# Performance work log

Measured on AMD Instinct MI355X. Metric: run time of the kernel, lower is better.

Reference implementation:

```python
import jax, jax.numpy as jnp
import numpy as np

B, N, F, K = 4096, 2048, 64, 64


def setup_inputs() -> dict:
    key = jax.random.key(0)
    k1, k2, k3, k4, k5 = jax.random.split(key, 5)
    X = jax.random.normal(k1, (B, N), dtype=jnp.float32)
    W = jax.random.normal(k2, (1, N), dtype=jnp.float32) * (1.0 / np.sqrt(N))
    b = jax.random.normal(k3, (1,), dtype=jnp.float32)
    vector = jax.random.normal(k4, (N, F, K), dtype=jnp.float32)
    feature2field = jax.random.randint(k5, (N,), 0, F, dtype=jnp.int32)
    return {"X": X, "W": W, "b": b, "vector": vector, "feature2field": feature2field}


def reference(X, W, b, vector, feature2field):
    # linear part: [B, 1]
    linear = X @ W.T + b
    # field-aware latent vector of feature i w.r.t. its own field: V[i] = vector[i, f2f[i]]  -> [N, K]
    V = vector[jnp.arange(vector.shape[0]), feature2field]
    # pairwise latent dot products S[i,j] = <V[i], V[j]>  -> [N, N]
    S = V @ V.T
    # Gram matrix over batch: P[i,j] = sum_b X[b,i] * X[b,j]  -> [N, N]
    P = X.T @ X
    # original loop accumulates sum over i<j and over batch of S[i,j] * X[:,i]*X[:,j],
    # then adds that scalar to every row of the linear output
    triu = jnp.triu(jnp.ones_like(S), k=1)
    interaction = jnp.sum(S * P * triu)
    return linear + interaction
```

## Files before the change

### kernel.cpp

```cpp
#include <hip/hip_runtime.h>

#define NB 4096
#define NN 2048
#define NF 64
#define NK 64

#define RPB   16
#define TPB   1024
#define NWAVE 16
#define CPW   (NN / NWAVE)
#define KS    (CPW / 32)
#define GRID  (NB / RPB)

typedef short bf16x8 __attribute__((ext_vector_type(8)));
typedef float f32x4  __attribute__((ext_vector_type(4)));

#define OFF_VGTH 0
#define OFF_VGTL (OFF_VGTH + NK * NN * 2)
#define OFF_VN   (OFF_VGTL + NK * NN * 2)
#define OFF_LINT (OFF_VN + NN * 4)
#define OFF_STOT (OFF_LINT + NB * 4)

__device__ inline unsigned short bf16_rtn(float f) {
    unsigned u = __float_as_uint(f);
    return (unsigned short)((u + 0x7fffu + ((u >> 16) & 1u)) >> 16);
}

__global__ __launch_bounds__(256) void k_prep(const float* __restrict__ vec,
                                              const int* __restrict__ f2f,
                                              unsigned short* __restrict__ VgTh,
                                              unsigned short* __restrict__ VgTl,
                                              float* __restrict__ vnorm,
                                              float* __restrict__ stot) {
    __shared__ unsigned short tH[64][72];
    __shared__ unsigned short tL[64][72];
    const int t  = threadIdx.x;
    const int i0 = blockIdx.x * 64;
    if (blockIdx.x == 0 && t == 0) *stot = 0.f;
    {
        const int il = t >> 2;
        const int sg = (t & 3) * 16;
        const int i  = i0 + il;
        const int f  = f2f[i];
        const float* p = vec + (size_t)i * (NF * NK) + (size_t)f * NK + sg;
        float nsum = 0.f;
        #pragma unroll
        for (int j4 = 0; j4 < 4; ++j4) {
            float4 v = *reinterpret_cast<const float4*>(p + j4 * 4);
            float vv[4] = {v.x, v.y, v.z, v.w};
            #pragma unroll
            for (int e = 0; e < 4; ++e) {
                float x = vv[e];
                nsum = fmaf(x, x, nsum);
                unsigned xb = __float_as_uint(x);
                float hf = __uint_as_float(xb & 0xffff0000u);
                int k = sg + j4 * 4 + e;
                tH[il][k] = (unsigned short)(xb >> 16);
                tL[il][k] = bf16_rtn(x - hf);
            }
        }
        nsum += __shfl_xor(nsum, 1, 64);
        nsum += __shfl_xor(nsum, 2, 64);
        if ((t & 3) == 0) vnorm[i] = nsum;
    }
    __syncthreads();
    {
        const int k  = t >> 2;
        const int is = (t & 3) * 16;
        unsigned short hb[16], lb[16];
        #pragma unroll
        for (int j = 0; j < 16; ++j) { hb[j] = tH[is + j][k]; lb[j] = tL[is + j][k]; }
        unsigned short* ph = VgTh + (size_t)k * NN + i0 + is;
        unsigned short* pl = VgTl + (size_t)k * NN + i0 + is;
        *reinterpret_cast<uint4*>(ph)     = *reinterpret_cast<uint4*>(hb);
        *reinterpret_cast<uint4*>(ph + 8) = *reinterpret_cast<uint4*>(hb + 8);
        *reinterpret_cast<uint4*>(pl)     = *reinterpret_cast<uint4*>(lb);
        *reinterpret_cast<uint4*>(pl + 8) = *reinterpret_cast<uint4*>(lb + 8);
    }
}

__global__ __launch_bounds__(TPB, 4) void k_main(const float* __restrict__ X,
                                                 const float* __restrict__ Wg,
                                                 const unsigned short* __restrict__ VgTh,
                                                 const unsigned short* __restrict__ VgTl,
                                                 const float* __restrict__ vn,
                                                 float* __restrict__ lint,
                                                 float* __restrict__ stot) {
    __shared__ float Tl[NWAVE * 1088];
    __shared__ float linW[NWAVE * 17];
    __shared__ float ddW[NWAVE * 17];
    __shared__ float rowRes[RPB];

    const int t    = threadIdx.x;
    const int w    = t >> 6;
    const int lane = t & 63;
    const int m    = lane & 15;
    const int quad = lane >> 4;
    const int r0   = blockIdx.x * RPB;
    const int row  = r0 + m;
    const int cw   = w * CPW;

    const float* xp = X  + (size_t)row * NN + cw + quad * 8;
    const float* wp = Wg + cw + quad * 8;
    const float* np = vn + cw + quad * 8;
    const unsigned short* bhp = VgTh + (size_t)m * NN + cw + quad * 8;
    const unsigned short* blp = VgTl + (size_t)m * NN + cw + quad * 8;

    f32x4 acc[4];
    #pragma unroll
    for (int nt = 0; nt < 4; ++nt)
        #pragma unroll
        for (int e = 0; e < 4; ++e) acc[nt][e] = 0.f;
    float lin = 0.f, dd = 0.f;

    #pragma unroll
    for (int s = 0; s < KS; ++s) {
        float4 xa = *reinterpret_cast<const float4*>(xp + s * 32);
        float4 xb = *reinterpret_cast<const float4*>(xp + s * 32 + 4);
        float4 wa = *reinterpret_cast<const float4*>(wp + s * 32);
        float4 wb = *reinterpret_cast<const float4*>(wp + s * 32 + 4);
        float4 na = *reinterpret_cast<const float4*>(np + s * 32);
        float4 nb = *reinterpret_cast<const float4*>(np + s * 32 + 4);

        float xs8[8] = {xa.x, xa.y, xa.z, xa.w, xb.x, xb.y, xb.z, xb.w};
        float ws8[8] = {wa.x, wa.y, wa.z, wa.w, wb.x, wb.y, wb.z, wb.w};
        float ns8[8] = {na.x, na.y, na.z, na.w, nb.x, nb.y, nb.z, nb.w};

        #pragma unroll
        for (int j = 0; j < 8; ++j) {
            lin = fmaf(xs8[j], ws8[j], lin);
            dd  = fmaf(xs8[j] * xs8[j], ns8[j], dd);
        }

        bf16x8 ah, al;
        #pragma unroll
        for (int j = 0; j < 8; ++j) {
            unsigned ub = __float_as_uint(xs8[j]);
            ah[j] = (short)(ub >> 16);
            float hf = __uint_as_float(ub & 0xffff0000u);
            al[j] = (short)bf16_rtn(xs8[j] - hf);
        }

        #pragma unroll
        for (int nt = 0; nt < 4; ++nt) {
            bf16x8 bh = *reinterpret_cast<const bf16x8*>(bhp + (size_t)nt * 16 * NN + s * 32);
            bf16x8 bl = *reinterpret_cast<const bf16x8*>(blp + (size_t)nt * 16 * NN + s * 32);
            acc[nt] = __builtin_amdgcn_mfma_f32_16x16x32_bf16(ah, bh, acc[nt], 0, 0, 0);
            acc[nt] = __builtin_amdgcn_mfma_f32_16x16x32_bf16(al, bh, acc[nt], 0, 0, 0);
            acc[nt] = __builtin_amdgcn_mfma_f32_16x16x32_bf16(ah, bl, acc[nt], 0, 0, 0);
        }
    }

    #pragma unroll
    for (int nt = 0; nt < 4; ++nt)
        #pragma unroll
        for (int r = 0; r < 4; ++r)
            Tl[w * 1088 + (quad * 4 + r) * 68 + nt * 16 + m] = acc[nt][r];

    lin += __shfl_xor(lin, 16, 64); lin += __shfl_xor(lin, 32, 64);
    dd  += __shfl_xor(dd, 16, 64);  dd  += __shfl_xor(dd, 32, 64);
    if (quad == 0) { linW[w * 17 + m] = lin; ddW[w * 17 + m] = dd; }
    __syncthreads();

    {
        float ts = 0.f;
        #pragma unroll
        for (int ww = 0; ww < NWAVE; ++ww)
            ts += Tl[ww * 1088 + w * 68 + lane];
        float s2 = ts * ts;
        #pragma unroll
        for (int d = 1; d < 64; d <<= 1) s2 += __shfl_xor(s2, d, 64);
        float lw = (lane < 16) ? linW[lane * 17 + w] : 0.f;
        float dw = (lane < 16) ? ddW [lane * 17 + w] : 0.f;
        #pragma unroll
        for (int d = 1; d < 16; d <<= 1) {
            lw += __shfl_xor(lw, d, 64);
            dw += __shfl_xor(dw, d, 64);
        }
        if (lane == 0) {
            lint[r0 + w] = lw;
            rowRes[w]    = s2 - dw;
        }
    }
    __syncthreads();

    if (t == 0) {
        float p = 0.f;
        #pragma unroll
        for (int r = 0; r < RPB; ++r) p += rowRes[r];
        atomicAdd(stot, p);
    }
}

__global__ __launch_bounds__(256) void k_final(const float* __restrict__ lint,
                                               const float* __restrict__ stot,
                                               const float* __restrict__ bptr,
                                               float* __restrict__ out) {
    int b = blockIdx.x * 256 + threadIdx.x;
    out[b] = lint[b] + bptr[0] + 0.5f * stot[0];
}

extern "C" void kernel_launch(void* const* d_in, const int* in_sizes, int n_in,
                              void* d_out, int out_size, void* d_ws, size_t ws_size,
                              hipStream_t stream) {
    const float* X    = (const float*)d_in[0];
    const float* W    = (const float*)d_in[1];
    const float* bias = (const float*)d_in[2];
    const float* vec  = (const float*)d_in[3];
    const int*   f2f  = (const int*)d_in[4];
    float* out = (float*)d_out;

    char* base = (char*)d_ws;
    unsigned short* VgTh = (unsigned short*)(base + OFF_VGTH);
    unsigned short* VgTl = (unsigned short*)(base + OFF_VGTL);
    float* vnorm = (float*)(base + OFF_VN);
    float* lint  = (float*)(base + OFF_LINT);
    float* stot  = (float*)(base + OFF_STOT);

    k_prep<<<NN / 64, 256, 0, stream>>>(vec, f2f, VgTh, VgTl, vnorm, stot);
    k_main<<<GRID, TPB, 0, stream>>>(X, W, VgTh, VgTl, vnorm, lint, stot);
    k_final<<<NB / 256, 256, 0, stream>>>(lint, stot, bias, out);
}
```

Baseline: 118.5 us.

## Pre-swizzle V into MFMA fragment layout so B-operand loads are contiguous

```diff
diff --git a/kernel.cpp b/kernel.cpp
--- a/kernel.cpp
+++ b/kernel.cpp
@@ -15,9 +15,8 @@
 typedef short bf16x8 __attribute__((ext_vector_type(8)));
 typedef float f32x4  __attribute__((ext_vector_type(4)));
 
-#define OFF_VGTH 0
-#define OFF_VGTL (OFF_VGTH + NK * NN * 2)
-#define OFF_VN   (OFF_VGTL + NK * NN * 2)
+#define OFF_VGF  0
+#define OFF_VN   (OFF_VGF + 64 * 8 * 512 * 2)
 #define OFF_LINT (OFF_VN + NN * 4)
 #define OFF_STOT (OFF_LINT + NB * 4)
 
@@ -28,8 +27,7 @@
 
 __global__ __launch_bounds__(256) void k_prep(const float* __restrict__ vec,
                                               const int* __restrict__ f2f,
-                                              unsigned short* __restrict__ VgTh,
-                                              unsigned short* __restrict__ VgTl,
+                                              unsigned short* __restrict__ VgF,
                                               float* __restrict__ vnorm,
                                               float* __restrict__ stot) {
     __shared__ unsigned short tH[64][72];
@@ -65,24 +63,28 @@
     }
     __syncthreads();
     {
-        const int k  = t >> 2;
-        const int is = (t & 3) * 16;
+        const int r   = t >> 2;
+        const int seg = t & 3;
+        const int S   = blockIdx.x * 2 + (seg >> 1);
+        const int q1  = (seg & 1) * 2;
         unsigned short hb[16], lb[16];
         #pragma unroll
-        for (int j = 0; j < 16; ++j) { hb[j] = tH[is + j][k]; lb[j] = tL[is + j][k]; }
-        unsigned short* ph = VgTh + (size_t)k * NN + i0 + is;
-        unsigned short* pl = VgTl + (size_t)k * NN + i0 + is;
-        *reinterpret_cast<uint4*>(ph)     = *reinterpret_cast<uint4*>(hb);
-        *reinterpret_cast<uint4*>(ph + 8) = *reinterpret_cast<uint4*>(hb + 8);
-        *reinterpret_cast<uint4*>(pl)     = *reinterpret_cast<uint4*>(lb);
-        *reinterpret_cast<uint4*>(pl + 8) = *reinterpret_cast<uint4*>(lb + 8);
+        for (int u = 0; u < 16; ++u) {
+            hb[u] = tH[seg * 16 + u][r];
+            lb[u] = tL[seg * 16 + u][r];
+        }
+        unsigned short* d = VgF + ((size_t)S * 8 + (r >> 4) * 2) * 512
+                                + ((r & 15) * 4 + q1) * 8;
+        *reinterpret_cast<uint4*>(d)            = *reinterpret_cast<uint4*>(hb);
+        *reinterpret_cast<uint4*>(d + 8)        = *reinterpret_cast<uint4*>(hb + 8);
+        *reinterpret_cast<uint4*>(d + 512)      = *reinterpret_cast<uint4*>(lb);
+        *reinterpret_cast<uint4*>(d + 512 + 8)  = *reinterpret_cast<uint4*>(lb + 8);
     }
 }
 
 __global__ __launch_bounds__(TPB, 4) void k_main(const float* __restrict__ X,
                                                  const float* __restrict__ Wg,
-                                                 const unsigned short* __restrict__ VgTh,
-                                                 const unsigned short* __restrict__ VgTl,
+                                                 const unsigned short* __restrict__ VgF,
                                                  const float* __restrict__ vn,
                                                  float* __restrict__ lint,
                                                  float* __restrict__ stot) {
@@ -103,8 +105,7 @@
     const float* xp = X  + (size_t)row * NN + cw + quad * 8;
     const float* wp = Wg + cw + quad * 8;
     const float* np = vn + cw + quad * 8;
-    const unsigned short* bhp = VgTh + (size_t)m * NN + cw + quad * 8;
-    const unsigned short* blp = VgTl + (size_t)m * NN + cw + quad * 8;
+    const unsigned short* bp = VgF + (size_t)(w * 4) * 4096 + (m * 4 + quad) * 8;
 
     f32x4 acc[4];
     #pragma unroll
@@ -141,10 +142,11 @@
             al[j] = (short)bf16_rtn(xs8[j] - hf);
         }
 
+        const unsigned short* bs = bp + (size_t)s * 4096;
         #pragma unroll
         for (int nt = 0; nt < 4; ++nt) {
-            bf16x8 bh = *reinterpret_cast<const bf16x8*>(bhp + (size_t)nt * 16 * NN + s * 32);
-            bf16x8 bl = *reinterpret_cast<const bf16x8*>(blp + (size_t)nt * 16 * NN + s * 32);
+            bf16x8 bh = *reinterpret_cast<const bf16x8*>(bs + nt * 1024);
+            bf16x8 bl = *reinterpret_cast<const bf16x8*>(bs + nt * 1024 + 512);
             acc[nt] = __builtin_amdgcn_mfma_f32_16x16x32_bf16(ah, bh, acc[nt], 0, 0, 0);
             acc[nt] = __builtin_amdgcn_mfma_f32_16x16x32_bf16(al, bh, acc[nt], 0, 0, 0);
             acc[nt] = __builtin_amdgcn_mfma_f32_16x16x32_bf16(ah, bl, acc[nt], 0, 0, 0);
@@ -211,13 +213,12 @@
     float* out = (float*)d_out;
 
     char* base = (char*)d_ws;
-    unsigned short* VgTh = (unsigned short*)(base + OFF_VGTH);
-    unsigned short* VgTl = (unsigned short*)(base + OFF_VGTL);
+    unsigned short* VgF = (unsigned short*)(base + OFF_VGF);
     float* vnorm = (float*)(base + OFF_VN);
     float* lint  = (float*)(base + OFF_LINT);
     float* stot  = (float*)(base + OFF_STOT);
 
-    k_prep<<<NN / 64, 256, 0, stream>>>(vec, f2f, VgTh, VgTl, vnorm, stot);
-    k_main<<<GRID, TPB, 0, stream>>>(X, W, VgTh, VgTl, vnorm, lint, stot);
+    k_prep<<<NN / 64, 256, 0, stream>>>(vec, f2f, VgF, vnorm, stot);
+    k_main<<<GRID, TPB, 0, stream>>>(X, W, VgF, vnorm, lint, stot);
     k_final<<<NB / 256, 256, 0, stream>>>(lint, stot, bias, out);
 }
```

Measured after the change: 111.6 us. 5.8% less time.
